# Performance work log

Measured on AMD Instinct MI355X. Metric: run time of the kernel, lower is better.

## Reference

```python
import jax, jax.numpy as jnp
import numpy as np

C = 1.0            # curvature for the single key 'A'
N_NODES = 100000
N_EDGES = 600000
D = 128
EPS = 1e-15
DEN_EPS = 1e-10


def _artanh(x):
    return jnp.arctanh(jnp.clip(x, -1.0 + 1e-7, 1.0 - 1e-7))


def _safe_norm(v):
    return jnp.clip(jnp.linalg.norm(v, axis=-1, keepdims=True), EPS)


def expmap0(u, c):
    sc = jnp.sqrt(c)
    un = _safe_norm(u)
    return jnp.tanh(sc * un) * u / (sc * un)


def logmap0(p, c):
    sc = jnp.sqrt(c)
    pn = _safe_norm(p)
    return _artanh(sc * pn) * p / (sc * pn)


def mobius_scalar_mul(r, v, c):
    sc = jnp.sqrt(c)
    vn = _safe_norm(v)
    return jnp.tanh(r * _artanh(sc * vn)) * v / (sc * vn)


def weighted_midpoint_spmm(x_hyp, c, rows, cols, vals):
    # Lorentz (conformal) factor gamma_i = 2 / (1 - c ||x_i||^2), shape [N, 1]
    gamma = 2.0 / jnp.clip(1.0 - c * jnp.sum(x_hyp * x_hyp, axis=-1, keepdims=True), EPS)
    gx = gamma * x_hyp                                   # [N, D]
    # sparse matmul via gather + segment-sum over destination rows
    num = jax.ops.segment_sum(vals[:, None] * gx[cols], rows, num_segments=N_NODES)      # [N, D]
    den = jax.ops.segment_sum(vals * (gamma[:, 0] - 1.0)[cols], rows, num_segments=N_NODES)[:, None]
    sign = jnp.where(den >= 0, 1.0, -1.0)
    den = sign * jnp.clip(jnp.abs(den), DEN_EPS)          # sign-preserving clamp_abs
    two_mean = num / den
    # gyromidpoint: 0.5 (x)_c two_mean
    return mobius_scalar_mul(0.5, two_mean, c)


def setup_inputs() -> dict:
    key = jax.random.key(0)
    k1, k2, k3, k4 = jax.random.split(key, 4)
    x = jax.random.normal(k1, (N_NODES, D), dtype=jnp.float32) * 0.05
    rows = jnp.sort(jax.random.randint(k2, (N_EDGES,), 0, N_NODES, dtype=jnp.int32))
    cols = jax.random.randint(k3, (N_EDGES,), 0, N_NODES, dtype=jnp.int32)
    vals = jax.random.uniform(k4, (N_EDGES,), dtype=jnp.float32)
    return {"x": x, "rows": rows, "cols": cols, "vals": vals}


def reference(x, rows, cols, vals):
    # hyper_agg for the single key 'A' of the c / adj dicts
    x_hyp = expmap0(x, C)
    x_hyp_agg = weighted_midpoint_spmm(x_hyp, C, rows, cols, vals)
    x_euc_agg = logmap0(x_hyp_agg, C)
    return x_euc_agg
```

## Files before the change

kernel.cpp:

```cpp
#include <hip/hip_runtime.h>
#include <math.h>

#define N_NODES_C 100000
#define N_EDGES_C 600000
#define NODES_PER_BLOCK_K1 8
#define ROWS_PER_BLOCK 16

static __device__ __forceinline__ unsigned short f2bf(float f) {
    unsigned int u = __float_as_uint(f);
    u += 0x7fffu + ((u >> 16) & 1u);
    return (unsigned short)(u >> 16);
}

__global__ void __launch_bounds__(256)
node_scale_kernel(const float4* __restrict__ x4,
                  ushort4* __restrict__ gxb,
                  float* __restrict__ gm1) {
    const int grp  = threadIdx.x >> 5;
    const int lane = threadIdx.x & 31;
    const int node = blockIdx.x * NODES_PER_BLOCK_K1 + grp;

    const float4 v = x4[(size_t)node * 32 + lane];
    float ss = v.x * v.x + v.y * v.y + v.z * v.z + v.w * v.w;
    #pragma unroll
    for (int m = 16; m > 0; m >>= 1) ss += __shfl_xor(ss, m, 64);

    const float un = fmaxf(sqrtf(ss), 1e-15f);
    const float e2 = __expf(2.0f * un);
    const float th = (e2 - 1.0f) / (e2 + 1.0f);
    const float gamma = 2.0f / fmaxf(1.0f - th * th, 1e-15f);
    const float s = gamma * th / un;

    ushort4 o;
    o.x = f2bf(s * v.x);
    o.y = f2bf(s * v.y);
    o.z = f2bf(s * v.z);
    o.w = f2bf(s * v.w);
    gxb[(size_t)node * 32 + lane] = o;
    if (lane == 0) gm1[node] = gamma - 1.0f;
}

__global__ void rowptr_kernel(const int* __restrict__ rows,
                              int* __restrict__ row_ptr) {
    const int i = blockIdx.x * blockDim.x + threadIdx.x;
    if (i > N_NODES_C) return;
    int lo = 0, hi = N_EDGES_C;
    while (lo < hi) {
        int mid = (lo + hi) >> 1;
        if (rows[mid] < i) lo = mid + 1; else hi = mid;
    }
    row_ptr[i] = lo;
}

static __device__ __forceinline__ void fma8(const uint4 u, const float w, float* a) {
    a[0] = fmaf(w, __uint_as_float(u.x << 16),          a[0]);
    a[1] = fmaf(w, __uint_as_float(u.x & 0xffff0000u),  a[1]);
    a[2] = fmaf(w, __uint_as_float(u.y << 16),          a[2]);
    a[3] = fmaf(w, __uint_as_float(u.y & 0xffff0000u),  a[3]);
    a[4] = fmaf(w, __uint_as_float(u.z << 16),          a[4]);
    a[5] = fmaf(w, __uint_as_float(u.z & 0xffff0000u),  a[5]);
    a[6] = fmaf(w, __uint_as_float(u.w << 16),          a[6]);
    a[7] = fmaf(w, __uint_as_float(u.w & 0xffff0000u),  a[7]);
}

__global__ void __launch_bounds__(256)
agg_kernel(const uint4* __restrict__ gxb,
           const float* __restrict__ gm1,
           const int* __restrict__ cols,
           const float* __restrict__ vals,
           const int* __restrict__ row_ptr,
           float4* __restrict__ out4) {
    const int grp  = threadIdx.x >> 4;
    const int lane = threadIdx.x & 15;
    const int row  = blockIdx.x * ROWS_PER_BLOCK + grp;

    const int e0  = row_ptr[row];
    const int deg = row_ptr[row + 1] - e0;

    float acc[8] = {0.f, 0.f, 0.f, 0.f, 0.f, 0.f, 0.f, 0.f};
    float den_l = 0.0f;

    for (int base = 0; base < deg; base += 16) {
        const int m = min(16, deg - base);
        int   myc = 0;
        float myw = 0.0f;
        if (lane < m) {
            const int e = e0 + base + lane;
            myc = cols[e];
            myw = vals[e];
            den_l = fmaf(myw, gm1[myc], den_l);
        }

        int j = 0;
        for (; j + 4 <= m; j += 4) {
            const int   c0 = __shfl(myc, j + 0, 16);
            const int   c1 = __shfl(myc, j + 1, 16);
            const int   c2 = __shfl(myc, j + 2, 16);
            const int   c3 = __shfl(myc, j + 3, 16);
            const float w0 = __shfl(myw, j + 0, 16);
            const float w1 = __shfl(myw, j + 1, 16);
            const float w2 = __shfl(myw, j + 2, 16);
            const float w3 = __shfl(myw, j + 3, 16);
            const uint4 v0 = gxb[(size_t)c0 * 16 + lane];
            const uint4 v1 = gxb[(size_t)c1 * 16 + lane];
            const uint4 v2 = gxb[(size_t)c2 * 16 + lane];
            const uint4 v3 = gxb[(size_t)c3 * 16 + lane];
            fma8(v0, w0, acc);
            fma8(v1, w1, acc);
            fma8(v2, w2, acc);
            fma8(v3, w3, acc);
        }
        if (j + 2 <= m) {
            const int   c0 = __shfl(myc, j + 0, 16);
            const int   c1 = __shfl(myc, j + 1, 16);
            const float w0 = __shfl(myw, j + 0, 16);
            const float w1 = __shfl(myw, j + 1, 16);
            const uint4 v0 = gxb[(size_t)c0 * 16 + lane];
            const uint4 v1 = gxb[(size_t)c1 * 16 + lane];
            fma8(v0, w0, acc);
            fma8(v1, w1, acc);
            j += 2;
        }
        if (j < m) {
            const int   c0 = __shfl(myc, j, 16);
            const float w0 = __shfl(myw, j, 16);
            const uint4 v0 = gxb[(size_t)c0 * 16 + lane];
            fma8(v0, w0, acc);
        }
    }

    float den = den_l;
    #pragma unroll
    for (int m = 8; m > 0; m >>= 1) den += __shfl_xor(den, m, 16);

    const float sden = (den >= 0.0f) ? 1.0f : -1.0f;
    den = sden * fmaxf(fabsf(den), 1e-10f);

    float t[8];
    float ssl = 0.0f;
    #pragma unroll
    for (int i = 0; i < 8; ++i) { t[i] = acc[i] / den; ssl = fmaf(t[i], t[i], ssl); }

    float ss = ssl;
    #pragma unroll
    for (int m = 8; m > 0; m >>= 1) ss += __shfl_xor(ss, m, 16);

    const float tn = sqrtf(ss);
    const float vn = fmaxf(tn, 1e-15f);
    const float ac = fminf(vn, 1.0f - 1e-7f);
    const float tanhval = ac / (1.0f + sqrtf(fmaxf(1.0f - ac * ac, 0.0f)));
    const float m_scale = tanhval / vn;
    const float pn = fmaxf(tanhval * (tn / vn), 1e-15f);
    const float pc = fminf(pn, 1.0f - 1e-7f);
    const float at = 0.5f * __logf((1.0f + pc) / (1.0f - pc));
    const float o_scale = (at / pn) * m_scale;

    float4 o0, o1;
    o0.x = o_scale * t[0]; o0.y = o_scale * t[1];
    o0.z = o_scale * t[2]; o0.w = o_scale * t[3];
    o1.x = o_scale * t[4]; o1.y = o_scale * t[5];
    o1.z = o_scale * t[6]; o1.w = o_scale * t[7];
    out4[(size_t)row * 32 + lane * 2 + 0] = o0;
    out4[(size_t)row * 32 + lane * 2 + 1] = o1;
}

extern "C" void kernel_launch(void* const* d_in, const int* in_sizes, int n_in,
                              void* d_out, int out_size, void* d_ws, size_t ws_size,
                              hipStream_t stream) {
    const float4* x4   = (const float4*)d_in[0];
    const int*    rows = (const int*)d_in[1];
    const int*    cols = (const int*)d_in[2];
    const float*  vals = (const float*)d_in[3];
    float4* out4 = (float4*)d_out;

    ushort4* gxb = (ushort4*)d_ws;
    float* gm1   = (float*)((char*)d_ws + (size_t)N_NODES_C * 128 * 2);
    int* row_ptr = (int*)(gm1 + N_NODES_C);

    node_scale_kernel<<<N_NODES_C / NODES_PER_BLOCK_K1, 256, 0, stream>>>(x4, gxb, gm1);
    rowptr_kernel<<<(N_NODES_C + 1 + 255) / 256, 256, 0, stream>>>(rows, row_ptr);
    agg_kernel<<<N_NODES_C / ROWS_PER_BLOCK, 256, 0, stream>>>((const uint4*)gxb, gm1, cols, vals, row_ptr, out4);
}
```

Before: 144.0 us.

## Quantize gathered node features to int8 with per-node scale and fuse rowptr

Stores the gamma-scaled node features as int8 with a per-node absmax scale instead of bf16, halving bytes gathered per edge in the aggregation kernel. The per-node scale is folded into the edge weight, and it is packed with gamma-1 into a float2. The row-pointer binary search is merged into the node scaling kernel to drop a launch. This trades accuracy (8-bit quantization error) for reduced gather bandwidth.

```diff
diff --git a/kernel.cpp b/kernel.cpp
--- a/kernel.cpp
+++ b/kernel.cpp
@@ -6,16 +6,22 @@
 #define NODES_PER_BLOCK_K1 8
 #define ROWS_PER_BLOCK 16
 
-static __device__ __forceinline__ unsigned short f2bf(float f) {
-    unsigned int u = __float_as_uint(f);
-    u += 0x7fffu + ((u >> 16) & 1u);
-    return (unsigned short)(u >> 16);
-}
-
 __global__ void __launch_bounds__(256)
 node_scale_kernel(const float4* __restrict__ x4,
-                  ushort4* __restrict__ gxb,
-                  float* __restrict__ gm1) {
+                  const int* __restrict__ rows,
+                  unsigned int* __restrict__ gxq,
+                  float2* __restrict__ sg,
+                  int* __restrict__ row_ptr) {
+    const int gid = blockIdx.x * blockDim.x + threadIdx.x;
+    if (gid <= N_NODES_C) {
+        int lo = 0, hi = N_EDGES_C;
+        while (lo < hi) {
+            int mid = (lo + hi) >> 1;
+            if (rows[mid] < gid) lo = mid + 1; else hi = mid;
+        }
+        row_ptr[gid] = lo;
+    }
+
     const int grp  = threadIdx.x >> 5;
     const int lane = threadIdx.x & 31;
     const int node = blockIdx.x * NODES_PER_BLOCK_K1 + grp;
@@ -31,41 +37,40 @@
     const float gamma = 2.0f / fmaxf(1.0f - th * th, 1e-15f);
     const float s = gamma * th / un;
 
-    ushort4 o;
-    o.x = f2bf(s * v.x);
-    o.y = f2bf(s * v.y);
-    o.z = f2bf(s * v.z);
-    o.w = f2bf(s * v.w);
-    gxb[(size_t)node * 32 + lane] = o;
-    if (lane == 0) gm1[node] = gamma - 1.0f;
+    float4 g;
+    g.x = s * v.x; g.y = s * v.y; g.z = s * v.z; g.w = s * v.w;
+
+    float amax = fmaxf(fmaxf(fabsf(g.x), fabsf(g.y)), fmaxf(fabsf(g.z), fabsf(g.w)));
+    #pragma unroll
+    for (int m = 16; m > 0; m >>= 1) amax = fmaxf(amax, __shfl_xor(amax, m, 64));
+
+    const float inv = (amax > 0.0f) ? (127.0f / amax) : 0.0f;
+    int q0 = (int)rintf(g.x * inv);
+    int q1 = (int)rintf(g.y * inv);
+    int q2 = (int)rintf(g.z * inv);
+    int q3 = (int)rintf(g.w * inv);
+    q0 = min(max(q0, -127), 127); q1 = min(max(q1, -127), 127);
+    q2 = min(max(q2, -127), 127); q3 = min(max(q3, -127), 127);
+    const unsigned int packed = (q0 & 0xff) | ((q1 & 0xff) << 8) |
+                                ((q2 & 0xff) << 16) | ((q3 & 0xff) << 24);
+    gxq[(size_t)node * 32 + lane] = packed;
+    if (lane == 0) sg[node] = make_float2(amax / 127.0f, gamma - 1.0f);
 }
 
-__global__ void rowptr_kernel(const int* __restrict__ rows,
-                              int* __restrict__ row_ptr) {
-    const int i = blockIdx.x * blockDim.x + threadIdx.x;
-    if (i > N_NODES_C) return;
-    int lo = 0, hi = N_EDGES_C;
-    while (lo < hi) {
-        int mid = (lo + hi) >> 1;
-        if (rows[mid] < i) lo = mid + 1; else hi = mid;
-    }
-    row_ptr[i] = lo;
-}
-
-static __device__ __forceinline__ void fma8(const uint4 u, const float w, float* a) {
-    a[0] = fmaf(w, __uint_as_float(u.x << 16),          a[0]);
-    a[1] = fmaf(w, __uint_as_float(u.x & 0xffff0000u),  a[1]);
-    a[2] = fmaf(w, __uint_as_float(u.y << 16),          a[2]);
-    a[3] = fmaf(w, __uint_as_float(u.y & 0xffff0000u),  a[3]);
-    a[4] = fmaf(w, __uint_as_float(u.z << 16),          a[4]);
-    a[5] = fmaf(w, __uint_as_float(u.z & 0xffff0000u),  a[5]);
-    a[6] = fmaf(w, __uint_as_float(u.w << 16),          a[6]);
-    a[7] = fmaf(w, __uint_as_float(u.w & 0xffff0000u),  a[7]);
+static __device__ __forceinline__ void fma8i(const uint2 u, const float ws, float* a) {
+    a[0] = fmaf(ws, (float)((int)(u.x << 24) >> 24), a[0]);
+    a[1] = fmaf(ws, (float)((int)(u.x << 16) >> 24), a[1]);
+    a[2] = fmaf(ws, (float)((int)(u.x <<  8) >> 24), a[2]);
+    a[3] = fmaf(ws, (float)((int) u.x        >> 24), a[3]);
+    a[4] = fmaf(ws, (float)((int)(u.y << 24) >> 24), a[4]);
+    a[5] = fmaf(ws, (float)((int)(u.y << 16) >> 24), a[5]);
+    a[6] = fmaf(ws, (float)((int)(u.y <<  8) >> 24), a[6]);
+    a[7] = fmaf(ws, (float)((int) u.y        >> 24), a[7]);
 }
 
 __global__ void __launch_bounds__(256)
-agg_kernel(const uint4* __restrict__ gxb,
-           const float* __restrict__ gm1,
+agg_kernel(const uint2* __restrict__ gxq,
+           const float2* __restrict__ sg,
            const int* __restrict__ cols,
            const float* __restrict__ vals,
            const int* __restrict__ row_ptr,
@@ -82,50 +87,52 @@
 
     for (int base = 0; base < deg; base += 16) {
         const int m = min(16, deg - base);
-        int   myc = 0;
-        float myw = 0.0f;
+        int   myc  = 0;
+        float myws = 0.0f;
         if (lane < m) {
             const int e = e0 + base + lane;
             myc = cols[e];
-            myw = vals[e];
-            den_l = fmaf(myw, gm1[myc], den_l);
+            const float w = vals[e];
+            const float2 s2 = sg[myc];
+            myws = w * s2.x;
+            den_l = fmaf(w, s2.y, den_l);
         }
 
         int j = 0;
         for (; j + 4 <= m; j += 4) {
-            const int   c0 = __shfl(myc, j + 0, 16);
-            const int   c1 = __shfl(myc, j + 1, 16);
-            const int   c2 = __shfl(myc, j + 2, 16);
-            const int   c3 = __shfl(myc, j + 3, 16);
-            const float w0 = __shfl(myw, j + 0, 16);
-            const float w1 = __shfl(myw, j + 1, 16);
-            const float w2 = __shfl(myw, j + 2, 16);
-            const float w3 = __shfl(myw, j + 3, 16);
-            const uint4 v0 = gxb[(size_t)c0 * 16 + lane];
-            const uint4 v1 = gxb[(size_t)c1 * 16 + lane];
-            const uint4 v2 = gxb[(size_t)c2 * 16 + lane];
-            const uint4 v3 = gxb[(size_t)c3 * 16 + lane];
-            fma8(v0, w0, acc);
-            fma8(v1, w1, acc);
-            fma8(v2, w2, acc);
-            fma8(v3, w3, acc);
+            const int   c0 = __shfl(myc,  j + 0, 16);
+            const int   c1 = __shfl(myc,  j + 1, 16);
+            const int   c2 = __shfl(myc,  j + 2, 16);
+            const int   c3 = __shfl(myc,  j + 3, 16);
+            const float w0 = __shfl(myws, j + 0, 16);
+            const float w1 = __shfl(myws, j + 1, 16);
+            const float w2 = __shfl(myws, j + 2, 16);
+            const float w3 = __shfl(myws, j + 3, 16);
+            const uint2 v0 = gxq[(size_t)c0 * 16 + lane];
+            const uint2 v1 = gxq[(size_t)c1 * 16 + lane];
+            const uint2 v2 = gxq[(size_t)c2 * 16 + lane];
+            const uint2 v3 = gxq[(size_t)c3 * 16 + lane];
+            fma8i(v0, w0, acc);
+            fma8i(v1, w1, acc);
+            fma8i(v2, w2, acc);
+            fma8i(v3, w3, acc);
         }
         if (j + 2 <= m) {
-            const int   c0 = __shfl(myc, j + 0, 16);
-            const int   c1 = __shfl(myc, j + 1, 16);
-            const float w0 = __shfl(myw, j + 0, 16);
-            const float w1 = __shfl(myw, j + 1, 16);
-            const uint4 v0 = gxb[(size_t)c0 * 16 + lane];
-            const uint4 v1 = gxb[(size_t)c1 * 16 + lane];
-            fma8(v0, w0, acc);
-            fma8(v1, w1, acc);
+            const int   c0 = __shfl(myc,  j + 0, 16);
+            const int   c1 = __shfl(myc,  j + 1, 16);
+            const float w0 = __shfl(myws, j + 0, 16);
+            const float w1 = __shfl(myws, j + 1, 16);
+            const uint2 v0 = gxq[(size_t)c0 * 16 + lane];
+            const uint2 v1 = gxq[(size_t)c1 * 16 + lane];
+            fma8i(v0, w0, acc);
+            fma8i(v1, w1, acc);
             j += 2;
         }
         if (j < m) {
-            const int   c0 = __shfl(myc, j, 16);
-            const float w0 = __shfl(myw, j, 16);
-            const uint4 v0 = gxb[(size_t)c0 * 16 + lane];
-            fma8(v0, w0, acc);
+            const int   c0 = __shfl(myc,  j, 16);
+            const float w0 = __shfl(myws, j, 16);
+            const uint2 v0 = gxq[(size_t)c0 * 16 + lane];
+            fma8i(v0, w0, acc);
         }
     }
 
@@ -173,11 +180,12 @@
     const float*  vals = (const float*)d_in[3];
     float4* out4 = (float4*)d_out;
 
-    ushort4* gxb = (ushort4*)d_ws;
-    float* gm1   = (float*)((char*)d_ws + (size_t)N_NODES_C * 128 * 2);
-    int* row_ptr = (int*)(gm1 + N_NODES_C);
+    unsigned int* gxq = (unsigned int*)d_ws;
+    float2* sg  = (float2*)((char*)d_ws + (size_t)N_NODES_C * 128);
+    int* row_ptr = (int*)(sg + N_NODES_C);
 
-    node_scale_kernel<<<N_NODES_C / NODES_PER_BLOCK_K1, 256, 0, stream>>>(x4, gxb, gm1);
-    rowptr_kernel<<<(N_NODES_C + 1 + 255) / 256, 256, 0, stream>>>(rows, row_ptr);
-    agg_kernel<<<N_NODES_C / ROWS_PER_BLOCK, 256, 0, stream>>>((const uint4*)gxb, gm1, cols, vals, row_ptr, out4);
+    node_scale_kernel<<<N_NODES_C / NODES_PER_BLOCK_K1, 256, 0, stream>>>(
+        x4, rows, gxq, sg, row_ptr);
+    agg_kernel<<<N_NODES_C / ROWS_PER_BLOCK, 256, 0, stream>>>(
+        (const uint2*)gxq, sg, cols, vals, row_ptr, out4);
 }
```

Result: faster. 132.4 us (-8.1%).
